# Performance work log

Measured on AMD Instinct MI355X. Metric: run time of the kernel, lower is better.

Reference implementation:

```python
import jax, jax.numpy as jnp
import numpy as np

B, S, IN, H = 16, 1024, 1024, 1024

def setup_inputs() -> dict:
    key = jax.random.key(0)
    k1, k2 = jax.random.split(key)
    x = jax.random.normal(k1, (B, S, IN), dtype=jnp.float32)
    # xavier_uniform with gain sqrt(2) over shape [2H, IN]
    limit = np.sqrt(2.0) * np.sqrt(6.0 / (2 * H + IN))
    W = jax.random.uniform(k2, (2 * H, IN), dtype=jnp.float32, minval=-limit, maxval=limit)
    return {"x": x, "W": W}

def reference(x, W):
    # i = x @ W.T -> [B, S, 2H]; split into key/value pre-activations
    i = jnp.einsum('bsi,oi->bso', x, W)
    ik, iv = jnp.split(i, 2, axis=2)          # each [B, S, H]
    mem0 = jnp.zeros((x.shape[0], H, H), dtype=x.dtype)

    def step(mem, kv):
        ik_t, iv_t = kv                        # [B, H] each
        k = jax.nn.relu(ik_t)
        v = jax.nn.relu(iv_t)
        # Hebbian plasticity rule: delta_mem = key outer val
        mem = mem + jnp.einsum('bk,bv->bkv', k, v)
        return mem, (k, v)

    # scan over time: move seq axis to front
    kv_seq = (jnp.swapaxes(ik, 0, 1), jnp.swapaxes(iv, 0, 1))  # [S, B, H]
    mem, (keys, vals) = jax.lax.scan(step, mem0, kv_seq)
    keys = jnp.swapaxes(keys, 0, 1)            # [B, S, H]
    vals = jnp.swapaxes(vals, 0, 1)
    return mem, keys, vals
```

## Files before the change

kernel.cpp:

```cpp
#include <hip/hip_runtime.h>

#define B_  16
#define S_  1024
#define IN_ 1024
#define H_  1024
#define N1  (2*H_)
#define M1  (B_*S_)
#define K1  IN_
#define XN  (M1*IN_)
#define WN  (N1*IN_)

#define BM  128
#define BN  128
#define BK  64
#define CP  130

typedef __attribute__((ext_vector_type(8))) short  short8;
typedef __attribute__((ext_vector_type(4))) float  floatx4;

__device__ __forceinline__ unsigned short f2bf(float f) {
    unsigned int u = __float_as_uint(f);
    u += 0x7fffu + ((u >> 16) & 1u);
    return (unsigned short)(u >> 16);
}

#define GLDS16(gp, lp) __builtin_amdgcn_global_load_lds(                      \
    (const __attribute__((address_space(1))) void*)(gp),                      \
    (__attribute__((address_space(3))) void*)(lp), 16, 0, 0)

__global__ __launch_bounds__(256) void convert_kernel(
    const float* __restrict__ x, const float* __restrict__ W,
    unsigned short* __restrict__ xb, unsigned short* __restrict__ Wb)
{
    size_t i = ((size_t)blockIdx.x * 256 + threadIdx.x) * 8;
    const float* src;
    unsigned short* dst;
    if (i < (size_t)XN) { src = x + i; dst = xb + i; }
    else                { src = W + (i - XN); dst = Wb + (i - XN); }
    float4 a = *(const float4*)(src);
    float4 b = *(const float4*)(src + 4);
    ushort4 p = { f2bf(a.x), f2bf(a.y), f2bf(a.z), f2bf(a.w) };
    ushort4 q = { f2bf(b.x), f2bf(b.y), f2bf(b.z), f2bf(b.w) };
    *(ushort4*)(dst)     = p;
    *(ushort4*)(dst + 4) = q;
}


__global__ __launch_bounds__(256) void gemm1_kernel(
    const unsigned short* __restrict__ xb, const unsigned short* __restrict__ Wb,
    float* __restrict__ out,
    unsigned short* __restrict__ kT, unsigned short* __restrict__ vT)
{
    __shared__ unsigned short lds[BM * CP];
    unsigned short* ldsA = lds;
    unsigned short* ldsB = lds + BM * BK;

    const int tid  = threadIdx.x;
    const int wave = tid >> 6, lane = tid & 63;
    const int quad = lane >> 4, r = lane & 15;
    const int wm = (wave >> 1) * 64;
    const int wn = (wave & 1) * 64;

    const int L    = blockIdx.x;
    const int xcd  = L & 7;
    const int s    = L >> 3;
    const int rect = (s >> 6) * 8 + xcd;
    const int idx  = s & 63;
    const int rm   = rect & 15, rc = rect >> 4;
    const int mt   = rm * 8 + (idx >> 3);
    const int nt   = rc * 8 + (idx & 7);
    const int m0   = mt * BM;
    const int n0   = nt * BN;

    const unsigned short* Ag = xb + (size_t)m0 * K1;
    const unsigned short* Bg = Wb + (size_t)n0 * K1;

    floatx4 acc[4][4] = {};

    for (int kt = 0; kt < K1; kt += BK) {
        __syncthreads();
#pragma unroll
        for (int t = 0; t < 4; ++t) {
            int seg  = t * 4 + wave;
            int slot = seg * 64 + lane;
            int row  = slot >> 3, c = slot & 7;
            int cs   = c ^ (row & 7);
            GLDS16(Ag + (size_t)row * K1 + kt + cs * 8, ldsA + seg * 512);
            GLDS16(Bg + (size_t)row * K1 + kt + cs * 8, ldsB + seg * 512);
        }
        __syncthreads();

#pragma unroll
        for (int sc = 0; sc < 2; ++sc) {
            short8 af[4], bfr[4];
            const int g = sc * 4 + quad;
#pragma unroll
            for (int i = 0; i < 4; ++i)
                af[i]  = *(const short8*)(ldsA + (wm + i * 16 + r) * BK + (g ^ (r & 7)) * 8);
#pragma unroll
            for (int j = 0; j < 4; ++j)
                bfr[j] = *(const short8*)(ldsB + (wn + j * 16 + r) * BK + (g ^ (r & 7)) * 8);
#pragma unroll
            for (int i = 0; i < 4; ++i)
#pragma unroll
                for (int j = 0; j < 4; ++j)
                    acc[i][j] = __builtin_amdgcn_mfma_f32_16x16x32_bf16(af[i], bfr[j], acc[i][j], 0, 0, 0);
        }
    }

    __syncthreads();
    unsigned short* ldsC = lds;

    const bool isKeys = (nt < 8);
    float* outKV    = out + (isKeys ? (size_t)M1 * H_ : (size_t)2 * M1 * H_);
    const int ncol0 = isKeys ? n0 : (n0 - 1024);

#pragma unroll
    for (int i = 0; i < 4; ++i)
#pragma unroll
        for (int j = 0; j < 4; ++j)
#pragma unroll
            for (int d = 0; d < 4; ++d) {
                int row_l = wm + i * 16 + quad * 4 + d;
                int col_l = wn + j * 16 + r;
                float v = fmaxf(acc[i][j][d], 0.0f);
                outKV[(size_t)(m0 + row_l) * H_ + ncol0 + col_l] = v;
                ldsC[row_l * CP + col_l] = f2bf(v);
            }
    __syncthreads();

    unsigned short* wsT = isKeys ? kT : vT;
    const int b  = m0 >> 10;
    const int s0 = m0 & 1023;
    unsigned short* dstBase = wsT + (size_t)b * H_ * S_ + (size_t)ncol0 * S_ + s0;
#pragma unroll
    for (int stp = 0; stp < 64; ++stp) {
        int o   = stp * 256 + tid;
        int n_l = o >> 7, m_l = o & 127;
        dstBase[(size_t)n_l * S_ + m_l] = ldsC[m_l * CP + n_l];
    }
}

__global__ __launch_bounds__(256) void gemm2_kernel(
    const unsigned short* __restrict__ kT, const unsigned short* __restrict__ vT,
    float* __restrict__ mem)
{
    __shared__ unsigned short lds[BM * BK * 2];
    unsigned short* ldsA = lds;
    unsigned short* ldsB = lds + BM * BK;

    const int tid  = threadIdx.x;
    const int wave = tid >> 6, lane = tid & 63;
    const int quad = lane >> 4, r = lane & 15;
    const int wm = (wave >> 1) * 64;
    const int wn = (wave & 1) * 64;

    const int L   = blockIdx.x;
    const int xcd = L & 7;
    const int s   = L >> 3;
    const int b   = xcd * 2 + (s >> 6);
    const int t   = s & 63;
    const int m0  = (t >> 3) * BM;
    const int n0  = (t & 7) * BN;

    const unsigned short* Ag = kT + (size_t)b * H_ * S_ + (size_t)m0 * S_;
    const unsigned short* Bg = vT + (size_t)b * H_ * S_ + (size_t)n0 * S_;

    floatx4 acc[4][4] = {};

    for (int kt = 0; kt < S_; kt += BK) {
        __syncthreads();
#pragma unroll
        for (int tt = 0; tt < 4; ++tt) {
            int seg  = tt * 4 + wave;
            int slot = seg * 64 + lane;
            int row  = slot >> 3, c = slot & 7;
            int cs   = c ^ (row & 7);
            GLDS16(Ag + (size_t)row * S_ + kt + cs * 8, ldsA + seg * 512);
            GLDS16(Bg + (size_t)row * S_ + kt + cs * 8, ldsB + seg * 512);
        }
        __syncthreads();

#pragma unroll
        for (int sc = 0; sc < 2; ++sc) {
            short8 af[4], bfr[4];
            const int g = sc * 4 + quad;
#pragma unroll
            for (int i = 0; i < 4; ++i)
                af[i]  = *(const short8*)(ldsA + (wm + i * 16 + r) * BK + (g ^ (r & 7)) * 8);
#pragma unroll
            for (int j = 0; j < 4; ++j)
                bfr[j] = *(const short8*)(ldsB + (wn + j * 16 + r) * BK + (g ^ (r & 7)) * 8);
#pragma unroll
            for (int i = 0; i < 4; ++i)
#pragma unroll
                for (int j = 0; j < 4; ++j)
                    acc[i][j] = __builtin_amdgcn_mfma_f32_16x16x32_bf16(af[i], bfr[j], acc[i][j], 0, 0, 0);
        }
    }

    float* outb = mem + (size_t)b * H_ * H_;
#pragma unroll
    for (int i = 0; i < 4; ++i)
#pragma unroll
        for (int j = 0; j < 4; ++j)
#pragma unroll
            for (int d = 0; d < 4; ++d) {
                int row_l = wm + i * 16 + quad * 4 + d;
                int col_l = wn + j * 16 + r;
                outb[(size_t)(m0 + row_l) * H_ + n0 + col_l] = acc[i][j][d];
            }
}

extern "C" void kernel_launch(void* const* d_in, const int* in_sizes, int n_in,
                              void* d_out, int out_size, void* d_ws, size_t ws_size,
                              hipStream_t stream) {
    const float* x = (const float*)d_in[0];
    const float* W = (const float*)d_in[1];
    float* out = (float*)d_out;

    unsigned short* xb = (unsigned short*)d_out;
    unsigned short* Wb = xb + (size_t)XN;

    unsigned short* kT = (unsigned short*)d_ws;
    unsigned short* vT = kT + (size_t)B_ * H_ * S_;

    convert_kernel<<<dim3((XN + WN) / 2048), dim3(256), 0, stream>>>(x, W, xb, Wb);

    gemm1_kernel<<<dim3(2048), dim3(256), 0, stream>>>(xb, Wb, out, kT, vT);

    gemm2_kernel<<<dim3(1024), dim3(256), 0, stream>>>(kT, vT, out);
}
```

Measured before the change: 364.4 us.

## Use 256x256 tiles with double-buffered LDS pipelining in both GEMMs

Both GEMMs move from 128x128 tiles with 4 waves and single-buffered LDS to 256x256 tiles with 8 waves and two 64KB LDS buffers. Global-to-LDS loads for the next k-step are interleaved with MFMA work on the current buffer, using sched barriers and setprio. The goal is higher arithmetic intensity and hiding load latency behind compute. The gemm1 transposed bf16 write is redone in two halves with ushort4 stores. The trade-off is fewer blocks (512 and 256) on a 256-CU part, plus more registers and LDS per block.

```diff
diff --git a/kernel.cpp b/kernel.cpp
--- a/kernel.cpp
+++ b/kernel.cpp
@@ -9,11 +9,12 @@
 #define K1  IN_
 #define XN  (M1*IN_)
 #define WN  (N1*IN_)
-
-#define BM  128
-#define BN  128
+#define LDG 1024
+
+#define BM  256
+#define BN  256
 #define BK  64
-#define CP  130
+#define CP  257
 
 typedef __attribute__((ext_vector_type(8))) short  short8;
 typedef __attribute__((ext_vector_type(4))) float  floatx4;
@@ -45,170 +46,188 @@
     *(ushort4*)(dst + 4) = q;
 }
 
-
-__global__ __launch_bounds__(256) void gemm1_kernel(
+__device__ __forceinline__ void stage_unit(
+    const unsigned short* Ag, const unsigned short* Bg,
+    unsigned short* lbuf, int u, int kt, int wave, int lane)
+{
+    const unsigned short* src = (u < 2) ? (Ag + (size_t)u * 128 * LDG)
+                                        : (Bg + (size_t)(u - 2) * 128 * LDG);
+    unsigned short* dstu = lbuf + ((u < 2) ? u * 8192 : 16384 + (u - 2) * 8192);
+#pragma unroll
+    for (int h = 0; h < 2; ++h) {
+        int e   = (wave * 2 + h) * 64 + lane;
+        int row = e >> 3, c = e & 7;
+        int cs  = c ^ (row & 7);
+        GLDS16(src + (size_t)row * LDG + kt + cs * 8, dstu + (wave * 2 + h) * 512);
+    }
+}
+
+__device__ __forceinline__ void gemm_core(
+    const unsigned short* Ag, const unsigned short* Bg,
+    unsigned short* lds, floatx4 (&acc)[8][4], int wave, int lane)
+{
+    const int quad = lane >> 4, r = lane & 15;
+    const int wmw  = (wave >> 2) * 128;
+    const int wnw  = (wave & 3) * 64;
+
+#pragma unroll
+    for (int u = 0; u < 4; ++u) stage_unit(Ag, Bg, lds, u, 0, wave, lane);
+
+    for (int t = 0; t < 16; ++t) {
+        unsigned short* bufc = lds + (t & 1) * 32768;
+        unsigned short* bufn = lds + ((t + 1) & 1) * 32768;
+        const int  ktn = (t + 1) * BK;
+        const bool st  = (t < 15);
+        __syncthreads();
+        const unsigned short* cA = bufc;
+        const unsigned short* cB = bufc + 16384;
+        short8 bfr[4];
+#pragma unroll
+        for (int kc = 0; kc < 2; ++kc)
+#pragma unroll
+        for (int mh = 0; mh < 2; ++mh) {
+            const int g = kc * 4 + quad;
+            short8 af[4];
+#pragma unroll
+            for (int i = 0; i < 4; ++i)
+                af[i] = *(const short8*)(cA + (wmw + (mh * 4 + i) * 16 + r) * BK
+                                            + (g ^ (r & 7)) * 8);
+            if (mh == 0) {
+#pragma unroll
+                for (int j = 0; j < 4; ++j)
+                    bfr[j] = *(const short8*)(cB + (wnw + j * 16 + r) * BK
+                                                 + (g ^ (r & 7)) * 8);
+            }
+            if (st) stage_unit(Ag, Bg, bufn, kc * 2 + mh, ktn, wave, lane);
+            __builtin_amdgcn_sched_barrier(0);
+            __builtin_amdgcn_s_barrier();
+            __builtin_amdgcn_s_setprio(1);
+#pragma unroll
+            for (int i = 0; i < 4; ++i)
+#pragma unroll
+                for (int j = 0; j < 4; ++j)
+                    acc[mh * 4 + i][j] = __builtin_amdgcn_mfma_f32_16x16x32_bf16(
+                        af[i], bfr[j], acc[mh * 4 + i][j], 0, 0, 0);
+            __builtin_amdgcn_s_setprio(0);
+            __builtin_amdgcn_sched_barrier(0);
+            if (kc + mh < 2) __builtin_amdgcn_s_barrier();
+        }
+    }
+    __syncthreads();
+}
+
+__global__ __launch_bounds__(512, 2) void gemm1_kernel(
     const unsigned short* __restrict__ xb, const unsigned short* __restrict__ Wb,
     float* __restrict__ out,
     unsigned short* __restrict__ kT, unsigned short* __restrict__ vT)
 {
-    __shared__ unsigned short lds[BM * CP];
-    unsigned short* ldsA = lds;
-    unsigned short* ldsB = lds + BM * BK;
+    __shared__ unsigned short lds[65536];
 
     const int tid  = threadIdx.x;
     const int wave = tid >> 6, lane = tid & 63;
     const int quad = lane >> 4, r = lane & 15;
-    const int wm = (wave >> 1) * 64;
-    const int wn = (wave & 1) * 64;
-
-    const int L    = blockIdx.x;
-    const int xcd  = L & 7;
-    const int s    = L >> 3;
-    const int rect = (s >> 6) * 8 + xcd;
-    const int idx  = s & 63;
-    const int rm   = rect & 15, rc = rect >> 4;
-    const int mt   = rm * 8 + (idx >> 3);
-    const int nt   = rc * 8 + (idx & 7);
-    const int m0   = mt * BM;
-    const int n0   = nt * BN;
+    const int wmw  = (wave >> 2) * 128;
+    const int wnw  = (wave & 3) * 64;
+
+    const int L   = blockIdx.x;
+    const int xcd = L & 7, s = L >> 3;
+    const int mt  = xcd * 8 + (s >> 3);
+    const int nt  = s & 7;
+    const int m0  = mt * BM, n0 = nt * BN;
 
     const unsigned short* Ag = xb + (size_t)m0 * K1;
     const unsigned short* Bg = Wb + (size_t)n0 * K1;
 
-    floatx4 acc[4][4] = {};
-
-    for (int kt = 0; kt < K1; kt += BK) {
-        __syncthreads();
-#pragma unroll
-        for (int t = 0; t < 4; ++t) {
-            int seg  = t * 4 + wave;
-            int slot = seg * 64 + lane;
-            int row  = slot >> 3, c = slot & 7;
-            int cs   = c ^ (row & 7);
-            GLDS16(Ag + (size_t)row * K1 + kt + cs * 8, ldsA + seg * 512);
-            GLDS16(Bg + (size_t)row * K1 + kt + cs * 8, ldsB + seg * 512);
-        }
-        __syncthreads();
-
-#pragma unroll
-        for (int sc = 0; sc < 2; ++sc) {
-            short8 af[4], bfr[4];
-            const int g = sc * 4 + quad;
-#pragma unroll
-            for (int i = 0; i < 4; ++i)
-                af[i]  = *(const short8*)(ldsA + (wm + i * 16 + r) * BK + (g ^ (r & 7)) * 8);
-#pragma unroll
-            for (int j = 0; j < 4; ++j)
-                bfr[j] = *(const short8*)(ldsB + (wn + j * 16 + r) * BK + (g ^ (r & 7)) * 8);
-#pragma unroll
-            for (int i = 0; i < 4; ++i)
-#pragma unroll
-                for (int j = 0; j < 4; ++j)
-                    acc[i][j] = __builtin_amdgcn_mfma_f32_16x16x32_bf16(af[i], bfr[j], acc[i][j], 0, 0, 0);
-        }
-    }
-
-    __syncthreads();
-    unsigned short* ldsC = lds;
-
-    const bool isKeys = (nt < 8);
+    floatx4 acc[8][4] = {};
+    gemm_core(Ag, Bg, lds, acc, wave, lane);
+
+    const bool isKeys = (nt < 4);
     float* outKV    = out + (isKeys ? (size_t)M1 * H_ : (size_t)2 * M1 * H_);
     const int ncol0 = isKeys ? n0 : (n0 - 1024);
 
 #pragma unroll
-    for (int i = 0; i < 4; ++i)
+    for (int f = 0; f < 8; ++f)
 #pragma unroll
         for (int j = 0; j < 4; ++j)
 #pragma unroll
             for (int d = 0; d < 4; ++d) {
-                int row_l = wm + i * 16 + quad * 4 + d;
-                int col_l = wn + j * 16 + r;
-                float v = fmaxf(acc[i][j][d], 0.0f);
-                outKV[(size_t)(m0 + row_l) * H_ + ncol0 + col_l] = v;
-                ldsC[row_l * CP + col_l] = f2bf(v);
+                int row_l = wmw + f * 16 + quad * 4 + d;
+                int col_l = wnw + j * 16 + r;
+                outKV[(size_t)(m0 + row_l) * H_ + ncol0 + col_l] =
+                    fmaxf(acc[f][j][d], 0.0f);
             }
-    __syncthreads();
 
     unsigned short* wsT = isKeys ? kT : vT;
     const int b  = m0 >> 10;
     const int s0 = m0 & 1023;
-    unsigned short* dstBase = wsT + (size_t)b * H_ * S_ + (size_t)ncol0 * S_ + s0;
-#pragma unroll
-    for (int stp = 0; stp < 64; ++stp) {
-        int o   = stp * 256 + tid;
-        int n_l = o >> 7, m_l = o & 127;
-        dstBase[(size_t)n_l * S_ + m_l] = ldsC[m_l * CP + n_l];
+    unsigned short* dstB = wsT + (size_t)b * H_ * S_ + (size_t)ncol0 * S_ + s0;
+
+#pragma unroll
+    for (int ch = 0; ch < 2; ++ch) {
+        if ((wave >> 2) == ch) {
+#pragma unroll
+            for (int f = 0; f < 8; ++f)
+#pragma unroll
+                for (int j = 0; j < 4; ++j)
+#pragma unroll
+                    for (int d = 0; d < 4; ++d) {
+                        int lrow = f * 16 + quad * 4 + d;
+                        int col  = wnw + j * 16 + r;
+                        lds[lrow * CP + col] = f2bf(fmaxf(acc[f][j][d], 0.0f));
+                    }
+        }
+        __syncthreads();
+#pragma unroll
+        for (int it = 0; it < 16; ++it) {
+            int o   = it * 512 + tid;
+            int n_l = o >> 5;
+            int m4  = (o & 31) * 4;
+            ushort4 v;
+            v.x = lds[(m4 + 0) * CP + n_l];
+            v.y = lds[(m4 + 1) * CP + n_l];
+            v.z = lds[(m4 + 2) * CP + n_l];
+            v.w = lds[(m4 + 3) * CP + n_l];
+            *(ushort4*)(dstB + (size_t)n_l * S_ + ch * 128 + m4) = v;
+        }
+        __syncthreads();
     }
 }
 
-__global__ __launch_bounds__(256) void gemm2_kernel(
+__global__ __launch_bounds__(512, 2) void gemm2_kernel(
     const unsigned short* __restrict__ kT, const unsigned short* __restrict__ vT,
     float* __restrict__ mem)
 {
-    __shared__ unsigned short lds[BM * BK * 2];
-    unsigned short* ldsA = lds;
-    unsigned short* ldsB = lds + BM * BK;
+    __shared__ unsigned short lds[65536];
 
     const int tid  = threadIdx.x;
     const int wave = tid >> 6, lane = tid & 63;
     const int quad = lane >> 4, r = lane & 15;
-    const int wm = (wave >> 1) * 64;
-    const int wn = (wave & 1) * 64;
+    const int wmw  = (wave >> 2) * 128;
+    const int wnw  = (wave & 3) * 64;
 
     const int L   = blockIdx.x;
-    const int xcd = L & 7;
-    const int s   = L >> 3;
-    const int b   = xcd * 2 + (s >> 6);
-    const int t   = s & 63;
-    const int m0  = (t >> 3) * BM;
-    const int n0  = (t & 7) * BN;
+    const int xcd = L & 7, s = L >> 3;
+    const int b   = xcd * 2 + (s >> 4);
+    const int tt  = s & 15;
+    const int m0  = (tt >> 2) * BM;
+    const int n0  = (tt & 3) * BN;
 
     const unsigned short* Ag = kT + (size_t)b * H_ * S_ + (size_t)m0 * S_;
     const unsigned short* Bg = vT + (size_t)b * H_ * S_ + (size_t)n0 * S_;
 
-    floatx4 acc[4][4] = {};
-
-    for (int kt = 0; kt < S_; kt += BK) {
-        __syncthreads();
-#pragma unroll
-        for (int tt = 0; tt < 4; ++tt) {
-            int seg  = tt * 4 + wave;
-            int slot = seg * 64 + lane;
-            int row  = slot >> 3, c = slot & 7;
-            int cs   = c ^ (row & 7);
-            GLDS16(Ag + (size_t)row * S_ + kt + cs * 8, ldsA + seg * 512);
-            GLDS16(Bg + (size_t)row * S_ + kt + cs * 8, ldsB + seg * 512);
-        }
-        __syncthreads();
-
-#pragma unroll
-        for (int sc = 0; sc < 2; ++sc) {
-            short8 af[4], bfr[4];
-            const int g = sc * 4 + quad;
-#pragma unroll
-            for (int i = 0; i < 4; ++i)
-                af[i]  = *(const short8*)(ldsA + (wm + i * 16 + r) * BK + (g ^ (r & 7)) * 8);
-#pragma unroll
-            for (int j = 0; j < 4; ++j)
-                bfr[j] = *(const short8*)(ldsB + (wn + j * 16 + r) * BK + (g ^ (r & 7)) * 8);
-#pragma unroll
-            for (int i = 0; i < 4; ++i)
-#pragma unroll
-                for (int j = 0; j < 4; ++j)
-                    acc[i][j] = __builtin_amdgcn_mfma_f32_16x16x32_bf16(af[i], bfr[j], acc[i][j], 0, 0, 0);
-        }
-    }
+    floatx4 acc[8][4] = {};
+    gemm_core(Ag, Bg, lds, acc, wave, lane);
 
     float* outb = mem + (size_t)b * H_ * H_;
 #pragma unroll
-    for (int i = 0; i < 4; ++i)
+    for (int f = 0; f < 8; ++f)
 #pragma unroll
         for (int j = 0; j < 4; ++j)
 #pragma unroll
             for (int d = 0; d < 4; ++d) {
-                int row_l = wm + i * 16 + quad * 4 + d;
-                int col_l = wn + j * 16 + r;
-                outb[(size_t)(m0 + row_l) * H_ + n0 + col_l] = acc[i][j][d];
+                int row_l = wmw + f * 16 + quad * 4 + d;
+                int col_l = wnw + j * 16 + r;
+                outb[(size_t)(m0 + row_l) * H_ + n0 + col_l] = acc[f][j][d];
             }
 }
 
@@ -227,7 +246,7 @@
 
     convert_kernel<<<dim3((XN + WN) / 2048), dim3(256), 0, stream>>>(x, W, xb, Wb);
 
-    gemm1_kernel<<<dim3(2048), dim3(256), 0, stream>>>(xb, Wb, out, kT, vT);
-
-    gemm2_kernel<<<dim3(1024), dim3(256), 0, stream>>>(kT, vT, out);
-}
+    gemm1_kernel<<<dim3(512), dim3(512), 0, stream>>>(xb, Wb, out, kT, vT);
+
+    gemm2_kernel<<<dim3(256), dim3(512), 0, stream>>>(kT, vT, out);
+}
```

Measured after the change: 349.4 us. 1.04x faster.
